# Optimization experiments

Hardware: AMD Instinct MI355X
Metric: run time of the kernel (lower is better)

The kernel has to match this reference:

```python
import jax, jax.numpy as jnp
import numpy as np

NUM_HEADS = 16


def rotate_half(x):
    # '... (j d) -> ... j d' with j=2: split last dim into two halves
    x1, x2 = jnp.split(x, 2, axis=-1)
    return jnp.concatenate([-x2, x1], axis=-1)


def apply_rotary_pos_emb(pos, t):
    # pos: [L, d] broadcast onto t: [B, H, L, d]
    return t * jnp.cos(pos) + rotate_half(t) * jnp.sin(pos)


def setup_inputs() -> dict:
    key = jax.random.key(0)
    ks = jax.random.split(key, 10)
    B, N, KV_N, C = 2, 2048, 2048, 1024
    hd = C // NUM_HEADS
    q = jax.random.normal(ks[0], (B, N, C), dtype=jnp.float32)
    k = jax.random.normal(ks[1], (B, KV_N, C), dtype=jnp.float32)
    v = jax.random.normal(ks[2], (B, KV_N, C), dtype=jnp.float32)
    mask = jax.random.randint(ks[3], (B, KV_N), 0, 2) > 0
    pos_emb = jax.random.normal(ks[4], (KV_N, hd), dtype=jnp.float32)
    s = 1.0 / np.sqrt(C)
    qW = jax.random.normal(ks[5], (C, C), dtype=jnp.float32) * s
    kW = jax.random.normal(ks[6], (C, C), dtype=jnp.float32) * s
    vW = jax.random.normal(ks[7], (C, C), dtype=jnp.float32) * s
    projW = jax.random.normal(ks[8], (C, C), dtype=jnp.float32) * s
    return {"q": q, "k": k, "v": v, "mask": mask, "pos_emb": pos_emb,
            "qW": qW, "kW": kW, "vW": vW, "projW": projW}


def reference(q, k, v, mask, pos_emb, qW, kW, vW, projW):
    B, N, C = q.shape
    H = NUM_HEADS
    hd = C // H
    scale = hd ** -0.5
    # linear projections (no bias)
    q = q @ qW
    k = k @ kW
    v = v @ vW
    # b l (h d) -> b h l d
    split = lambda t: t.reshape(t.shape[0], t.shape[1], H, hd).transpose(0, 2, 1, 3)
    q, k, v = split(q), split(k), split(v)
    q = q * scale
    # inline RoPE on q and k
    q = apply_rotary_pos_emb(pos_emb[:q.shape[-2]], q)
    k = apply_rotary_pos_emb(pos_emb[:k.shape[-2]], k)
    attn = jnp.einsum('bhid,bhjd->bhij', q, k)
    mask_value = -jnp.finfo(attn.dtype).max
    attn = jnp.where(mask[:, None, None, :], attn, mask_value)
    attn = jax.nn.softmax(attn, axis=-1)
    x = jnp.einsum('bhij,bhjd->bhid', attn, v)
    x = x.transpose(0, 2, 1, 3).reshape(B, N, C)
    return x @ projW
```

## Files before the change

kernel.cpp:

```cpp
#include <hip/hip_runtime.h>
#include <hip/hip_bf16.h>

#define BB 2
#define NN 2048
#define KVN 2048
#define CC 1024
#define HH 16
#define HD 64

typedef __bf16 bf16;
typedef __attribute__((ext_vector_type(4))) __bf16 bf16x4;
typedef __attribute__((ext_vector_type(8))) __bf16 bf16x8;
typedef __attribute__((ext_vector_type(4))) float f32x4;

__device__ __forceinline__ void gload_lds16(const void* g, void* l) {
  __builtin_amdgcn_global_load_lds(
      (const __attribute__((address_space(1))) void*)g,
      (__attribute__((address_space(3))) void*)l, 16, 0, 0);
}

__device__ __forceinline__ float exp2_raw(float x) {
  float r;
  asm("v_exp_f32 %0, %1" : "=v"(r) : "v"(x));
  return r;
}

__global__ __launch_bounds__(256)
void wtrans(const float* __restrict__ qW, const float* __restrict__ kW,
            const float* __restrict__ vW, const float* __restrict__ pW,
            bf16* __restrict__ Wt) {
  __shared__ bf16 t[64][72];
  const float* in = (blockIdx.z == 0) ? qW : (blockIdx.z == 1) ? kW
                    : (blockIdx.z == 2) ? vW : pW;
  bf16* out = Wt + (size_t)blockIdx.z * CC * CC;
  int r0 = blockIdx.y * 64, c0 = blockIdx.x * 64;
  int tid = threadIdx.x;
  int lr = tid >> 3, lc = (tid & 7) * 8;
  for (int p = 0; p < 2; ++p) {
    int rr = lr + p * 32;
    const float* src = &in[(size_t)(r0 + rr) * CC + c0 + lc];
    float4 a = *(const float4*)src;
    float4 b = *(const float4*)(src + 4);
    t[lc + 0][rr] = (bf16)a.x; t[lc + 1][rr] = (bf16)a.y;
    t[lc + 2][rr] = (bf16)a.z; t[lc + 3][rr] = (bf16)a.w;
    t[lc + 4][rr] = (bf16)b.x; t[lc + 5][rr] = (bf16)b.y;
    t[lc + 6][rr] = (bf16)b.z; t[lc + 7][rr] = (bf16)b.w;
  }
  __syncthreads();
  for (int p = 0; p < 2; ++p) {
    int rr = lr + p * 32;
    *(bf16x8*)&out[(size_t)(c0 + rr) * CC + r0 + lc] = *(const bf16x8*)&t[rr][lc];
  }
}

__global__ __launch_bounds__(256)
void cvt_qkv(const float* __restrict__ qin, const float* __restrict__ kin,
             const float* __restrict__ vin, bf16* __restrict__ Abf) {
  const int z = blockIdx.y;
  const float* s = (z == 0) ? qin : (z == 1) ? kin : vin;
  size_t off = ((size_t)blockIdx.x * 256 + threadIdx.x) * 8;
  float4 a = *(const float4*)(s + off);
  float4 b = *(const float4*)(s + off + 4);
  bf16x8 t;
  t[0] = (bf16)a.x; t[1] = (bf16)a.y; t[2] = (bf16)a.z; t[3] = (bf16)a.w;
  t[4] = (bf16)b.x; t[5] = (bf16)b.y; t[6] = (bf16)b.z; t[7] = (bf16)b.w;
  *(bf16x8*)&Abf[(size_t)z * ((size_t)BB * NN * CC) + off] = t;
}

__global__ __launch_bounds__(256, 3)
void gemm_qkv(const bf16* __restrict__ Abf, const bf16* __restrict__ Wt,
              const float* __restrict__ pos, bf16* __restrict__ Qp,
              bf16* __restrict__ Kpack, bf16* __restrict__ Vp) {
  __shared__ bf16 As[128 * 64];
  __shared__ bf16 Bs[128 * 64];
  const int bid = blockIdx.x;
  const int u = bid & 7, s = bid >> 3;
  const int nblk = s >> 2;
  const int m0 = (u * 4 + (s & 3)) * 128;
  const int z = nblk >> 3;
  const int n0 = (nblk & 7) * 128;
  const bf16* A = Abf + (size_t)z * ((size_t)BB * NN * CC);
  const bf16* Bt = Wt + (size_t)z * CC * CC;
  const int tid = threadIdx.x;
  const int wave = tid >> 6, lane = tid & 63;
  const int quad = lane >> 4, l15 = lane & 15;
  const int waveM = (wave >> 1) * 64, waveN = (wave & 1) * 64;
  f32x4 acc[4][4] = {};

  for (int k0 = 0; k0 < CC; k0 += 64) {
#pragma unroll
    for (int p = 0; p < 4; ++p) {
      int ch = p * 256 + tid;
      int r = ch >> 3, c = (ch & 7) ^ (r & 7);
      gload_lds16(Bt + (size_t)(n0 + r) * CC + k0 + c * 8, &Bs[ch * 8]);
    }
#pragma unroll
    for (int p = 0; p < 4; ++p) {
      int ch = p * 256 + tid;
      int r = ch >> 3, c = (ch & 7) ^ (r & 7);
      gload_lds16(A + (size_t)(m0 + r) * CC + k0 + c * 8, &As[ch * 8]);
    }
    __syncthreads();
    bf16x8 af[4][2], bfr[4][2];
#pragma unroll
    for (int i = 0; i < 4; ++i) {
      int rA = waveM + i * 16 + l15;
      af[i][0] = *(const bf16x8*)&As[(rA * 8 + (quad ^ (rA & 7))) * 8];
      af[i][1] = *(const bf16x8*)&As[(rA * 8 + ((quad + 4) ^ (rA & 7))) * 8];
      int rB = waveN + i * 16 + l15;
      bfr[i][0] = *(const bf16x8*)&Bs[(rB * 8 + (quad ^ (rB & 7))) * 8];
      bfr[i][1] = *(const bf16x8*)&Bs[(rB * 8 + ((quad + 4) ^ (rB & 7))) * 8];
    }
#pragma unroll
    for (int mi = 0; mi < 4; ++mi)
#pragma unroll
      for (int ni = 0; ni < 4; ++ni) {
        acc[mi][ni] = __builtin_amdgcn_mfma_f32_16x16x32_bf16(
            af[mi][0], bfr[ni][0], acc[mi][ni], 0, 0, 0);
        acc[mi][ni] = __builtin_amdgcn_mfma_f32_16x16x32_bf16(
            af[mi][1], bfr[ni][1], acc[mi][ni], 0, 0, 0);
      }
    __syncthreads();
  }
  const float scale = (z == 0) ? 0.125f * 1.44269504f : 1.0f;
  const int h2 = (n0 + waveN) >> 6;
#pragma unroll
  for (int mi = 0; mi < 4; ++mi) {
#pragma unroll
    for (int r = 0; r < 4; ++r) {
      int m = m0 + waveM + mi * 16 + quad * 4 + r;
      int l = m & (NN - 1);
      if (z == 2) {
#pragma unroll
        for (int ni = 0; ni < 4; ++ni)
          Vp[(size_t)m * CC + n0 + waveN + ni * 16 + l15] = (bf16)acc[mi][ni][r];
      } else if (z == 0) {
#pragma unroll
        for (int ni = 0; ni < 2; ++ni) {
          int col = n0 + waveN + ni * 16 + l15;
          int d = ni * 16 + l15;
          float x1 = acc[mi][ni][r], x2 = acc[mi][ni + 2][r];
          float s1, c1, s2f, c2f;
          __sincosf(pos[l * HD + d], &s1, &c1);
          __sincosf(pos[l * HD + d + 32], &s2f, &c2f);
          Qp[(size_t)m * CC + col]      = (bf16)((x1 * c1 - x2 * s1) * scale);
          Qp[(size_t)m * CC + col + 32] = (bf16)((x2 * c2f + x1 * s2f) * scale);
        }
      } else {
        int key = l;
        int bb2 = m >> 11;
        size_t kb_ = ((((size_t)(bb2 * HH + h2)) * 32 + (key >> 6)) * 8
                      + ((key >> 4) & 3) * 2) * 512 + (size_t)(key & 15) * 8;
#pragma unroll
        for (int ni = 0; ni < 2; ++ni) {
          int d = ni * 16 + l15;
          float x1 = acc[mi][ni][r], x2 = acc[mi][ni + 2][r];
          float s1, c1, s2f, c2f;
          __sincosf(pos[l * HD + d], &s1, &c1);
          __sincosf(pos[l * HD + d + 32], &s2f, &c2f);
          size_t off = kb_ + ((d >> 3) & 3) * 128 + (d & 7);
          Kpack[off]       = (bf16)(x1 * c1 - x2 * s1);
          Kpack[off + 512] = (bf16)(x2 * c2f + x1 * s2f);
        }
      }
    }
  }
}

__global__ __launch_bounds__(256)
void vpack_kernel(const bf16* __restrict__ Vp, const int* __restrict__ mask,
                  bf16* __restrict__ VpA, bf16* __restrict__ VpB) {
  __shared__ bf16 t[64][80];
  int tix = blockIdx.x, h = blockIdx.y, b = blockIdx.z;
  int j0 = tix * 64, bh = b * HH + h;
  const int* maskb = mask + b * KVN;
  int tid = threadIdx.x;
  int lr = tid >> 3, lc = (tid & 7) * 8;
  for (int p = 0; p < 2; ++p) {
    int j = lr + p * 32;
    int mv = maskb[j0 + j];
    bf16x8 v = *(const bf16x8*)&Vp[(size_t)(b * KVN + j0 + j) * CC + h * HD + lc];
#pragma unroll
    for (int uu = 0; uu < 8; ++uu) t[lc + uu][j] = mv ? v[uu] : (bf16)0.f;
  }
  __syncthreads();
  for (int p = 0; p < 3; ++p) {
    int sp = p * 256 + tid;
    if (sp < 640) {
      int fs = sp >> 6, lane = sp & 63, quad = (sp >> 4) & 3, l15 = sp & 15;
      int ni = fs >> 1, hf = fs & 1;
      bf16x8 v;
      if (ni < 4) {
        v = *(const bf16x8*)&t[ni * 16 + l15][hf * 32 + quad * 8];
      } else {
#pragma unroll
        for (int jj = 0; jj < 8; ++jj)
          v[jj] = (l15 == 0) ? (bf16)(float)maskb[j0 + hf * 32 + quad * 8 + jj]
                             : (bf16)0.f;
      }
      bf16* dst = (fs < 6) ? (VpA + (size_t)fs * (1 << 19))
                           : (VpB + (size_t)(fs - 6) * (1 << 19));
      *(bf16x8*)&dst[((size_t)(bh * 32 + tix)) * 512 + lane * 8] = v;
    }
  }
}

__global__ __launch_bounds__(256, 2)
void attn3(const bf16* __restrict__ Qp, const bf16* __restrict__ Kpack,
           const bf16* __restrict__ VpA, const bf16* __restrict__ VpB,
           bf16* __restrict__ X) {
  __shared__ char smem[49152];
  const int tid = threadIdx.x, wave = tid >> 6, lane = tid & 63;
  const int quad = lane >> 4, l15 = lane & 15;
  const int bid = blockIdx.x;
  const int u = bid & 7, s = bid >> 3;
  const int bh = u * 4 + (s & 3), qp = s >> 2;
  const int b = bh >> 4, h = bh & 15;
  const int qc = qp * 2 + (wave >> 1), kh = wave & 1;
  const int q0 = qc * 64;
  const int sw = 2 * (l15 & 7);

  bf16* P = (bf16*)(smem + wave * 2048);
  float* mrg = (float*)(smem + 8192);

  bf16x8 qa[4][2];
#pragma unroll
  for (int g = 0; g < 4; ++g) {
    const bf16* qrow = Qp + ((size_t)(b * NN) + q0 + g * 16 + l15) * CC + h * HD;
    qa[g][0] = *(const bf16x8*)&qrow[quad * 8];
    qa[g][1] = *(const bf16x8*)&qrow[32 + quad * 8];
  }

  f32x4 Oacc[4][5] = {};
  const bf16* kbase = Kpack + (size_t)bh * 32 * 8 * 512;

  for (int it = 0; it < 16; ++it) {
    int t = kh * 16 + it;
    bf16x8 kb[8], vb[10];
#pragma unroll
    for (int fs = 0; fs < 8; ++fs)
      kb[fs] = *(const bf16x8*)&kbase[((size_t)t * 8 + fs) * 512 + lane * 8];
#pragma unroll
    for (int fs = 0; fs < 10; ++fs) {
      const bf16* vbs = (fs < 6) ? (VpA + (size_t)fs * (1 << 19))
                                 : (VpB + (size_t)(fs - 6) * (1 << 19));
      vb[fs] = *(const bf16x8*)&vbs[((size_t)(bh * 32 + t)) * 512 + lane * 8];
    }
#pragma unroll
    for (int g = 0; g < 4; ++g) {
      f32x4 sg[4];
      __builtin_amdgcn_s_setprio(1);
#pragma unroll
      for (int ni = 0; ni < 4; ++ni) {
        f32x4 zz = {};
        zz = __builtin_amdgcn_mfma_f32_16x16x32_bf16(kb[ni * 2], qa[g][0], zz, 0, 0, 0);
        zz = __builtin_amdgcn_mfma_f32_16x16x32_bf16(kb[ni * 2 + 1], qa[g][1], zz, 0, 0, 0);
        sg[ni] = zz;
      }
      __builtin_amdgcn_s_setprio(0);
#pragma unroll
      for (int ni = 0; ni < 4; ++ni) {
        bf16x4 pk;
#pragma unroll
        for (int r = 0; r < 4; ++r) pk[r] = (bf16)exp2_raw(sg[ni][r] - 5.7707802f);
        *(bf16x4*)&P[(l15 * 16 + ((ni * 4 + quad) ^ sw)) * 4] = pk;
      }
      bf16x8 pf0 = *(const bf16x8*)&P[(l15 * 16 + ((quad * 2) ^ sw)) * 4];
      bf16x8 pf1 = *(const bf16x8*)&P[(l15 * 16 + ((8 + quad * 2) ^ sw)) * 4];
      __builtin_amdgcn_s_setprio(1);
#pragma unroll
      for (int ni = 0; ni < 5; ++ni) {
        Oacc[g][ni] = __builtin_amdgcn_mfma_f32_16x16x32_bf16(vb[ni * 2], pf0, Oacc[g][ni], 0, 0, 0);
        Oacc[g][ni] = __builtin_amdgcn_mfma_f32_16x16x32_bf16(vb[ni * 2 + 1], pf1, Oacc[g][ni], 0, 0, 0);
      }
      __builtin_amdgcn_s_setprio(0);
    }
  }
  if (kh == 1) {
    float* dst = mrg + (wave >> 1) * 5120 + lane * 4;
#pragma unroll
    for (int g = 0; g < 4; ++g)
#pragma unroll
      for (int ni = 0; ni < 5; ++ni)
        *(f32x4*)&dst[(g * 5 + ni) * 256] = Oacc[g][ni];
  }
  __syncthreads();
  if (kh == 0) {
    float* src = mrg + (wave >> 1) * 5120 + lane * 4;
#pragma unroll
    for (int g = 0; g < 4; ++g) {
#pragma unroll
      for (int ni = 0; ni < 5; ++ni) {
        f32x4 o = *(const f32x4*)&src[(g * 5 + ni) * 256];
#pragma unroll
        for (int r = 0; r < 4; ++r) Oacc[g][ni][r] += o[r];
      }
      float ls = __shfl(Oacc[g][4][0], l15, 64);
      float rn = 1.0f / ls;
#pragma unroll
      for (int ni = 0; ni < 4; ++ni) {
        bf16x4 ov;
#pragma unroll
        for (int r = 0; r < 4; ++r) ov[r] = (bf16)(Oacc[g][ni][r] * rn);
        *(bf16x4*)&X[((size_t)(b * NN) + q0 + g * 16 + l15) * CC
                     + h * HD + ni * 16 + quad * 4] = ov;
      }
    }
  }
}

__global__ __launch_bounds__(256, 4)
void gemm_proj(const bf16* __restrict__ A, const bf16* __restrict__ Bt,
               float* __restrict__ Out) {
  __shared__ bf16 As[64 * 64];
  __shared__ bf16 Bs[128 * 64];
  const int bid = blockIdx.x;
  const int u = bid & 7, s = bid >> 3;
  const int m0 = (u * 8 + (s >> 3)) * 64;
  const int n0 = (s & 7) * 128;
  const int tid = threadIdx.x;
  const int wave = tid >> 6, lane = tid & 63;
  const int quad = lane >> 4, l15 = lane & 15;
  const int waveM = (wave >> 1) * 32, waveN = (wave & 1) * 64;
  f32x4 acc[2][4] = {};

  for (int k0 = 0; k0 < CC; k0 += 64) {
#pragma unroll
    for (int p = 0; p < 2; ++p) {
      int ch = p * 256 + tid;
      int r = ch >> 3, c = (ch & 7) ^ (r & 7);
      gload_lds16(A + (size_t)(m0 + r) * CC + k0 + c * 8, &As[ch * 8]);
    }
#pragma unroll
    for (int p = 0; p < 4; ++p) {
      int ch = p * 256 + tid;
      int r = ch >> 3, c = (ch & 7) ^ (r & 7);
      gload_lds16(Bt + (size_t)(n0 + r) * CC + k0 + c * 8, &Bs[ch * 8]);
    }
    __syncthreads();
    bf16x8 af[2][2], bfr[4][2];
#pragma unroll
    for (int i = 0; i < 2; ++i) {
      int rA = waveM + i * 16 + l15;
      af[i][0] = *(const bf16x8*)&As[(rA * 8 + (quad ^ (rA & 7))) * 8];
      af[i][1] = *(const bf16x8*)&As[(rA * 8 + ((quad + 4) ^ (rA & 7))) * 8];
    }
#pragma unroll
    for (int i = 0; i < 4; ++i) {
      int rB = waveN + i * 16 + l15;
      bfr[i][0] = *(const bf16x8*)&Bs[(rB * 8 + (quad ^ (rB & 7))) * 8];
      bfr[i][1] = *(const bf16x8*)&Bs[(rB * 8 + ((quad + 4) ^ (rB & 7))) * 8];
    }
#pragma unroll
    for (int mi = 0; mi < 2; ++mi)
#pragma unroll
      for (int ni = 0; ni < 4; ++ni) {
        acc[mi][ni] = __builtin_amdgcn_mfma_f32_16x16x32_bf16(
            af[mi][0], bfr[ni][0], acc[mi][ni], 0, 0, 0);
        acc[mi][ni] = __builtin_amdgcn_mfma_f32_16x16x32_bf16(
            af[mi][1], bfr[ni][1], acc[mi][ni], 0, 0, 0);
      }
    __syncthreads();
  }
#pragma unroll
  for (int mi = 0; mi < 2; ++mi)
#pragma unroll
    for (int ni = 0; ni < 4; ++ni)
#pragma unroll
      for (int r = 0; r < 4; ++r) {
        int row = m0 + waveM + mi * 16 + quad * 4 + r;
        int col = n0 + waveN + ni * 16 + l15;
        Out[(size_t)row * CC + col] = acc[mi][ni][r];
      }
}

extern "C" void kernel_launch(void* const* d_in, const int* in_sizes, int n_in,
                              void* d_out, int out_size, void* d_ws, size_t ws_size,
                              hipStream_t stream) {
  const float* q    = (const float*)d_in[0];
  const float* k    = (const float*)d_in[1];
  const float* v    = (const float*)d_in[2];
  const int*   mask = (const int*)d_in[3];
  const float* pos  = (const float*)d_in[4];
  const float* qW   = (const float*)d_in[5];
  const float* kW   = (const float*)d_in[6];
  const float* vW   = (const float*)d_in[7];
  const float* pW   = (const float*)d_in[8];
  float* out = (float*)d_out;

  char* w = (char*)d_ws;
  const size_t MB = 1024 * 1024;
  bf16* Wt    = (bf16*)(w);
  bf16* Qp    = (bf16*)(w + 8 * MB);
  bf16* Kpack = (bf16*)(w + 16 * MB);
  bf16* Vp    = (bf16*)(w + 24 * MB);
  bf16* Abf   = (bf16*)(w + 32 * MB);
  bf16* VpA   = (bf16*)(w);
  bf16* VpB   = (bf16*)(w + 40 * MB);
  bf16* X     = (bf16*)(w + 32 * MB);

  wtrans<<<dim3(16, 16, 4), 256, 0, stream>>>(qW, kW, vW, pW, Wt);
  cvt_qkv<<<dim3(2048, 3), 256, 0, stream>>>(q, k, v, Abf);
  gemm_qkv<<<dim3(768), 256, 0, stream>>>(Abf, Wt, pos, Qp, Kpack, Vp);
  vpack_kernel<<<dim3(KVN / 64, HH, BB), 256, 0, stream>>>(Vp, mask, VpA, VpB);
  attn3<<<dim3(512), 256, 0, stream>>>(Qp, Kpack, VpA, VpB, X);
  gemm_proj<<<dim3(512), 256, 0, stream>>>(X, Wt + 3 * (size_t)CC * CC, out);
}
```

Before: 218.1 us.

## Fuse V masking and MFMA-fragment packing into QKV GEMM epilogue

The V projection epilogue now applies the key mask and writes V directly in the fragment-packed layout consumed by the attention kernel, along with the mask-row fragments. This removes the separate vpack kernel, the intermediate row-major V buffer, and its extra global-memory round trip and launch. The V epilogue issues scattered 8-byte stores instead of coalesced row stores, and the workspace layout changes to fit the new buffers.

```diff
diff --git a/kernel.cpp b/kernel.cpp
--- a/kernel.cpp
+++ b/kernel.cpp
@@ -69,8 +69,9 @@
 
 __global__ __launch_bounds__(256, 3)
 void gemm_qkv(const bf16* __restrict__ Abf, const bf16* __restrict__ Wt,
-              const float* __restrict__ pos, bf16* __restrict__ Qp,
-              bf16* __restrict__ Kpack, bf16* __restrict__ Vp) {
+              const float* __restrict__ pos, const int* __restrict__ mask,
+              bf16* __restrict__ Qp, bf16* __restrict__ Kpack,
+              bf16* __restrict__ Vpk, bf16* __restrict__ Mrow) {
   __shared__ bf16 As[128 * 64];
   __shared__ bf16 Bs[128 * 64];
   const int bid = blockIdx.x;
@@ -124,90 +125,86 @@
   }
   const float scale = (z == 0) ? 0.125f * 1.44269504f : 1.0f;
   const int h2 = (n0 + waveN) >> 6;
-#pragma unroll
-  for (int mi = 0; mi < 4; ++mi) {
-#pragma unroll
-    for (int r = 0; r < 4; ++r) {
-      int m = m0 + waveM + mi * 16 + quad * 4 + r;
-      int l = m & (NN - 1);
-      if (z == 2) {
-#pragma unroll
-        for (int ni = 0; ni < 4; ++ni)
-          Vp[(size_t)m * CC + n0 + waveN + ni * 16 + l15] = (bf16)acc[mi][ni][r];
-      } else if (z == 0) {
-#pragma unroll
-        for (int ni = 0; ni < 2; ++ni) {
-          int col = n0 + waveN + ni * 16 + l15;
-          int d = ni * 16 + l15;
-          float x1 = acc[mi][ni][r], x2 = acc[mi][ni + 2][r];
-          float s1, c1, s2f, c2f;
-          __sincosf(pos[l * HD + d], &s1, &c1);
-          __sincosf(pos[l * HD + d + 32], &s2f, &c2f);
-          Qp[(size_t)m * CC + col]      = (bf16)((x1 * c1 - x2 * s1) * scale);
-          Qp[(size_t)m * CC + col + 32] = (bf16)((x2 * c2f + x1 * s2f) * scale);
+  if (z == 2) {
+    const int row0 = m0 + waveM;
+    const int b2 = row0 >> 11;
+    const int tixl = (row0 & (NN - 1)) >> 6;
+    const int j0 = tixl * 64;
+    const int bh = b2 * HH + h2;
+    const int* maskb = mask + b2 * KVN;
+    const size_t tb = (size_t)(bh * 32 + tixl) * 512;
+#pragma unroll
+    for (int mi = 0; mi < 4; ++mi) {
+      int kl0 = mi * 16 + quad * 4;
+      int mv0 = maskb[j0 + kl0 + 0], mv1 = maskb[j0 + kl0 + 1];
+      int mv2 = maskb[j0 + kl0 + 2], mv3 = maskb[j0 + kl0 + 3];
+      int hf = mi >> 1;
+      int lane_v = ((mi & 1) * 2 + (quad >> 1)) * 16 + l15;
+      int jj0 = (quad & 1) * 4;
+#pragma unroll
+      for (int ni = 0; ni < 4; ++ni) {
+        int fs = ni * 2 + hf;
+        bf16x4 ov;
+        ov[0] = mv0 ? (bf16)acc[mi][ni][0] : (bf16)0.f;
+        ov[1] = mv1 ? (bf16)acc[mi][ni][1] : (bf16)0.f;
+        ov[2] = mv2 ? (bf16)acc[mi][ni][2] : (bf16)0.f;
+        ov[3] = mv3 ? (bf16)acc[mi][ni][3] : (bf16)0.f;
+        *(bf16x4*)&Vpk[(size_t)fs * (1 << 19) + tb + lane_v * 8 + jj0] = ov;
+      }
+    }
+#pragma unroll
+    for (int hf = 0; hf < 2; ++hf) {
+      bf16x8 mv;
+#pragma unroll
+      for (int jj = 0; jj < 8; ++jj)
+        mv[jj] = (l15 == 0) ? (bf16)(float)maskb[j0 + hf * 32 + quad * 8 + jj]
+                            : (bf16)0.f;
+      *(bf16x8*)&Mrow[(size_t)hf * (1 << 19) + tb + lane * 8] = mv;
+    }
+  } else {
+#pragma unroll
+    for (int mi = 0; mi < 4; ++mi) {
+#pragma unroll
+      for (int r = 0; r < 4; ++r) {
+        int m = m0 + waveM + mi * 16 + quad * 4 + r;
+        int l = m & (NN - 1);
+        if (z == 0) {
+#pragma unroll
+          for (int ni = 0; ni < 2; ++ni) {
+            int col = n0 + waveN + ni * 16 + l15;
+            int d = ni * 16 + l15;
+            float x1 = acc[mi][ni][r], x2 = acc[mi][ni + 2][r];
+            float s1, c1, s2f, c2f;
+            __sincosf(pos[l * HD + d], &s1, &c1);
+            __sincosf(pos[l * HD + d + 32], &s2f, &c2f);
+            Qp[(size_t)m * CC + col]      = (bf16)((x1 * c1 - x2 * s1) * scale);
+            Qp[(size_t)m * CC + col + 32] = (bf16)((x2 * c2f + x1 * s2f) * scale);
+          }
+        } else {
+          int key = l;
+          int bb2 = m >> 11;
+          size_t kb_ = ((((size_t)(bb2 * HH + h2)) * 32 + (key >> 6)) * 8
+                        + ((key >> 4) & 3) * 2) * 512 + (size_t)(key & 15) * 8;
+#pragma unroll
+          for (int ni = 0; ni < 2; ++ni) {
+            int d = ni * 16 + l15;
+            float x1 = acc[mi][ni][r], x2 = acc[mi][ni + 2][r];
+            float s1, c1, s2f, c2f;
+            __sincosf(pos[l * HD + d], &s1, &c1);
+            __sincosf(pos[l * HD + d + 32], &s2f, &c2f);
+            size_t off = kb_ + ((d >> 3) & 3) * 128 + (d & 7);
+            Kpack[off]       = (bf16)(x1 * c1 - x2 * s1);
+            Kpack[off + 512] = (bf16)(x2 * c2f + x1 * s2f);
+          }
         }
-      } else {
-        int key = l;
-        int bb2 = m >> 11;
-        size_t kb_ = ((((size_t)(bb2 * HH + h2)) * 32 + (key >> 6)) * 8
-                      + ((key >> 4) & 3) * 2) * 512 + (size_t)(key & 15) * 8;
-#pragma unroll
-        for (int ni = 0; ni < 2; ++ni) {
-          int d = ni * 16 + l15;
-          float x1 = acc[mi][ni][r], x2 = acc[mi][ni + 2][r];
-          float s1, c1, s2f, c2f;
-          __sincosf(pos[l * HD + d], &s1, &c1);
-          __sincosf(pos[l * HD + d + 32], &s2f, &c2f);
-          size_t off = kb_ + ((d >> 3) & 3) * 128 + (d & 7);
-          Kpack[off]       = (bf16)(x1 * c1 - x2 * s1);
-          Kpack[off + 512] = (bf16)(x2 * c2f + x1 * s2f);
-        }
-      }
-    }
-  }
-}
-
-__global__ __launch_bounds__(256)
-void vpack_kernel(const bf16* __restrict__ Vp, const int* __restrict__ mask,
-                  bf16* __restrict__ VpA, bf16* __restrict__ VpB) {
-  __shared__ bf16 t[64][80];
-  int tix = blockIdx.x, h = blockIdx.y, b = blockIdx.z;
-  int j0 = tix * 64, bh = b * HH + h;
-  const int* maskb = mask + b * KVN;
-  int tid = threadIdx.x;
-  int lr = tid >> 3, lc = (tid & 7) * 8;
-  for (int p = 0; p < 2; ++p) {
-    int j = lr + p * 32;
-    int mv = maskb[j0 + j];
-    bf16x8 v = *(const bf16x8*)&Vp[(size_t)(b * KVN + j0 + j) * CC + h * HD + lc];
-#pragma unroll
-    for (int uu = 0; uu < 8; ++uu) t[lc + uu][j] = mv ? v[uu] : (bf16)0.f;
-  }
-  __syncthreads();
-  for (int p = 0; p < 3; ++p) {
-    int sp = p * 256 + tid;
-    if (sp < 640) {
-      int fs = sp >> 6, lane = sp & 63, quad = (sp >> 4) & 3, l15 = sp & 15;
-      int ni = fs >> 1, hf = fs & 1;
-      bf16x8 v;
-      if (ni < 4) {
-        v = *(const bf16x8*)&t[ni * 16 + l15][hf * 32 + quad * 8];
-      } else {
-#pragma unroll
-        for (int jj = 0; jj < 8; ++jj)
-          v[jj] = (l15 == 0) ? (bf16)(float)maskb[j0 + hf * 32 + quad * 8 + jj]
-                             : (bf16)0.f;
-      }
-      bf16* dst = (fs < 6) ? (VpA + (size_t)fs * (1 << 19))
-                           : (VpB + (size_t)(fs - 6) * (1 << 19));
-      *(bf16x8*)&dst[((size_t)(bh * 32 + tix)) * 512 + lane * 8] = v;
+      }
     }
   }
 }
 
 __global__ __launch_bounds__(256, 2)
 void attn3(const bf16* __restrict__ Qp, const bf16* __restrict__ Kpack,
-           const bf16* __restrict__ VpA, const bf16* __restrict__ VpB,
+           const bf16* __restrict__ Vpk, const bf16* __restrict__ Mrow,
            bf16* __restrict__ X) {
   __shared__ char smem[49152];
   const int tid = threadIdx.x, wave = tid >> 6, lane = tid & 63;
@@ -242,8 +239,8 @@
       kb[fs] = *(const bf16x8*)&kbase[((size_t)t * 8 + fs) * 512 + lane * 8];
 #pragma unroll
     for (int fs = 0; fs < 10; ++fs) {
-      const bf16* vbs = (fs < 6) ? (VpA + (size_t)fs * (1 << 19))
-                                 : (VpB + (size_t)(fs - 6) * (1 << 19));
+      const bf16* vbs = (fs < 8) ? (Vpk + (size_t)fs * (1 << 19))
+                                 : (Mrow + (size_t)(fs - 8) * (1 << 19));
       vb[fs] = *(const bf16x8*)&vbs[((size_t)(bh * 32 + t)) * 512 + lane * 8];
     }
 #pragma unroll
@@ -393,16 +390,14 @@
   bf16* Wt    = (bf16*)(w);
   bf16* Qp    = (bf16*)(w + 8 * MB);
   bf16* Kpack = (bf16*)(w + 16 * MB);
-  bf16* Vp    = (bf16*)(w + 24 * MB);
+  bf16* Vpk   = (bf16*)(w + 24 * MB);
   bf16* Abf   = (bf16*)(w + 32 * MB);
-  bf16* VpA   = (bf16*)(w);
-  bf16* VpB   = (bf16*)(w + 40 * MB);
+  bf16* Mrow  = (bf16*)(w + 56 * MB);
   bf16* X     = (bf16*)(w + 32 * MB);
 
   wtrans<<<dim3(16, 16, 4), 256, 0, stream>>>(qW, kW, vW, pW, Wt);
   cvt_qkv<<<dim3(2048, 3), 256, 0, stream>>>(q, k, v, Abf);
-  gemm_qkv<<<dim3(768), 256, 0, stream>>>(Abf, Wt, pos, Qp, Kpack, Vp);
-  vpack_kernel<<<dim3(KVN / 64, HH, BB), 256, 0, stream>>>(Vp, mask, VpA, VpB);
-  attn3<<<dim3(512), 256, 0, stream>>>(Qp, Kpack, VpA, VpB, X);
+  gemm_qkv<<<dim3(768), 256, 0, stream>>>(Abf, Wt, pos, mask, Qp, Kpack, Vpk, Mrow);
+  attn3<<<dim3(512), 256, 0, stream>>>(Qp, Kpack, Vpk, Mrow, X);
   gemm_proj<<<dim3(512), 256, 0, stream>>>(X, Wt + 3 * (size_t)CC * CC, out);
 }
```

Measured after the change: 208.5 us. 4.4% less time.
